# Optimization experiments

Hardware: AMD Instinct MI355X
Metric: run time of the kernel (lower is better)

The kernel has to match this reference:

```python
import jax, jax.numpy as jnp
import numpy as np

HEADS = 4


def rel_to_abs(x):
    """Convert relative logits [..., L, 2L-1] to absolute [..., L, L].
    out[..., i, j] = x[..., i, j - i + L - 1]."""
    L = x.shape[-2]
    idx = jnp.arange(L)[None, :] - jnp.arange(L)[:, None] + (L - 1)  # [L, L]
    idx = jnp.broadcast_to(idx, x.shape[:-1] + (L,))
    return jnp.take_along_axis(x, idx, axis=-1)


def setup_inputs() -> dict:
    key = jax.random.key(0)
    ks = jax.random.split(key, 5)
    b, c, h, w = 2, 256, 64, 64
    dh = c // HEADS
    return {
        "x": jax.random.normal(ks[0], (b, c, h, w), jnp.float32),
        "w_qkv": jax.random.normal(ks[1], (3 * c, c), jnp.float32) / np.float32(np.sqrt(c)),
        "w_out": jax.random.normal(ks[2], (c, c), jnp.float32) / np.float32(np.sqrt(c)),
        "rel_height": jax.random.normal(ks[3], (2 * h - 1, dh), jnp.float32),
        "rel_width": jax.random.normal(ks[4], (2 * w - 1, dh), jnp.float32),
    }


def reference(x, w_qkv, w_out, rel_height, rel_width):
    b, c, h, w = x.shape
    dh = c // HEADS
    N = h * w
    scale = dh ** -0.5

    # 1x1 conv == per-pixel matmul over channels
    qkv = jnp.einsum('bchw,oc->bohw', x, w_qkv)  # [b, 3c, h, w]
    q, k, v = jnp.split(qkv, 3, axis=1)

    def to_heads(t):  # [b, c, h, w] -> [b, H, N, dh]
        return t.reshape(b, HEADS, dh, N).transpose(0, 1, 3, 2)

    q = to_heads(q) * scale
    k = to_heads(k)
    v = to_heads(v)

    # content-content scores over spatial positions
    content = jnp.einsum('bnid,bnjd->bnij', q, k)  # [b, H, N, N]

    q5 = q.reshape(b, HEADS, h, w, dh)  # [b, H, x, y, dh]
    # width relative logits: [b,H,x,y,2w-1] -> abs -> [b,H,x,y,jw]
    rw = rel_to_abs(jnp.einsum('bnxyd,rd->bnxyr', q5, rel_width))
    # height relative logits on transposed spatial: [b,H,y,x,2h-1] -> [b,H,y,x,jh]
    rh = rel_to_abs(jnp.einsum('bnyxd,rd->bnyxr', q5.transpose(0, 1, 3, 2, 4), rel_height))

    logits = content.reshape(b, HEADS, h, w, h, w)
    logits = logits + rw[:, :, :, :, None, :]  # broadcast width bias over target height jh
    logits = logits + rh.transpose(0, 1, 3, 2, 4)[:, :, :, :, :, None]  # [b,H,x,y,jh] over jw

    attn = jax.nn.softmax(logits.reshape(b, HEADS, N, N), axis=-1)
    out = jnp.einsum('bnij,bnjd->bnid', attn, v)  # [b, H, N, dh]
    out = out.transpose(0, 1, 3, 2).reshape(b, c, h, w)
    out = jnp.einsum('bchw,oc->bohw', out, w_out)  # 1x1 out projection
    return out + x
```

## Files before the change

### kernel.cpp

```cpp
#include <hip/hip_runtime.h>

typedef unsigned short u16;
typedef unsigned int u32;
typedef __bf16 bf16x8 __attribute__((ext_vector_type(8)));
typedef __bf16 bf16x2 __attribute__((ext_vector_type(2)));
typedef float f32x4 __attribute__((ext_vector_type(4)));
typedef float f32x2 __attribute__((ext_vector_type(2)));
typedef u32 u32x4 __attribute__((ext_vector_type(4)));
typedef u32 u32x2 __attribute__((ext_vector_type(2)));

#define DEVI __device__ __forceinline__

#if defined(__has_builtin)
#if __has_builtin(__builtin_amdgcn_exp2f)
#define EXP2F(x) __builtin_amdgcn_exp2f(x)
#endif
#endif
#ifndef EXP2F
#define EXP2F(x) exp2f(x)
#endif

#define MFMA16(a, b, c) __builtin_amdgcn_mfma_f32_16x16x32_bf16(a, b, c, 0, 0, 0)

typedef __attribute__((address_space(1))) u32 gu32;
typedef __attribute__((address_space(3))) u32 lu32;
DEVI void gll16(const u16* g, u16* l) {
    __builtin_amdgcn_global_load_lds((const gu32*)g, (lu32*)l, 16, 0, 0);
}
#define WAIT_VM0() __builtin_amdgcn_s_waitcnt(0x0f70)

DEVI u16 f2bf(float f) {
    u32 u = __builtin_bit_cast(u32, f);
    u = (u + 0x7FFFu + ((u >> 16) & 1u)) >> 16;
    return (u16)u;
}
DEVI float bf2f(u16 h) {
    u32 u = ((u32)h) << 16;
    return __builtin_bit_cast(float, u);
}
DEVI float bfhi(u32 u) { return __builtin_bit_cast(float, u & 0xFFFF0000u); }
DEVI float bflo(u32 u) { return __builtin_bit_cast(float, u << 16); }
DEVI bf16x8 bc8(u32x4 u) { return __builtin_bit_cast(bf16x8, u); }
DEVI u32 pack2(float a, float b) {
    f32x2 v = {a, b};
    bf16x2 h = __builtin_convertvector(v, bf16x2);
    return __builtin_bit_cast(u32, h);
}

#define QSCALE 0.18033688011112042f

__global__ __launch_bounds__(256) void k_prep(const float* __restrict__ x,
                                              const float* __restrict__ wq,
                                              const float* __restrict__ wo,
                                              const float* __restrict__ relh,
                                              const float* __restrict__ relw,
                                              u16* __restrict__ xt, u16* __restrict__ wqb,
                                              u16* __restrict__ wob, u16* __restrict__ relhb,
                                              u16* __restrict__ relwb) {
    int bid = blockIdx.x;
    int t = threadIdx.x;
    if (bid < 512) {
        int pm = bid & 63, cm = (bid >> 6) & 3, b = bid >> 8;
        int p0 = pm * 64, c0 = cm * 64;
        __shared__ float tile[64][65];
#pragma unroll
        for (int it = 0; it < 4; ++it) {
            int idx = it * 256 + t;
            int cl = idx >> 4, f4 = idx & 15;
            f32x4 v = *(const f32x4*)(x + ((size_t)(b * 256 + c0 + cl)) * 4096 + p0 + f4 * 4);
            tile[cl][f4 * 4 + 0] = v[0];
            tile[cl][f4 * 4 + 1] = v[1];
            tile[cl][f4 * 4 + 2] = v[2];
            tile[cl][f4 * 4 + 3] = v[3];
        }
        __syncthreads();
#pragma unroll
        for (int it = 0; it < 2; ++it) {
            int idx = it * 256 + t;
            int pl = idx >> 3, g = idx & 7;
            u32x4 pk;
            pk.x = pack2(tile[g * 8 + 0][pl], tile[g * 8 + 1][pl]);
            pk.y = pack2(tile[g * 8 + 2][pl], tile[g * 8 + 3][pl]);
            pk.z = pack2(tile[g * 8 + 4][pl], tile[g * 8 + 5][pl]);
            pk.w = pack2(tile[g * 8 + 6][pl], tile[g * 8 + 7][pl]);
            *(u32x4*)(xt + ((size_t)(b * 4096 + p0 + pl)) * 256 + c0 + g * 8) = pk;
        }
    } else {
        int i0 = (bid - 512) * 256 + t;
#pragma unroll
        for (int i = i0; i < 196608; i += 65536) wqb[i] = f2bf(wq[i]);
        if (i0 < 65536) wob[i0] = f2bf(wo[i0]);
        if (i0 < 8192) {
            relhb[i0] = (i0 < 8128) ? f2bf(relh[i0]) : (u16)0;
            relwb[i0] = (i0 < 8128) ? f2bf(relw[i0]) : (u16)0;
        }
    }
}

__global__ __launch_bounds__(256) void k_qkv(const u16* __restrict__ xt, const u16* __restrict__ wqb,
                                             const u16* __restrict__ relwb,
                                             const u16* __restrict__ relhb,
                                             u16* __restrict__ q, u16* __restrict__ k,
                                             u16* __restrict__ vt, u16* __restrict__ Wabs,
                                             u16* __restrict__ HabsT) {
    int pm = blockIdx.x, on = blockIdx.y, b = blockIdx.z;
    int p0 = pm * 64, o0 = on * 64;
    __shared__ __align__(16) u16 Sm[64 * 256];
    int t = threadIdx.x;
    int wv = t >> 6, l = t & 63, quad = l >> 4, li = l & 15;

    u32x4 areg[8];
    const u32x4* arow = (const u32x4*)(xt + ((size_t)(b * 4096 + p0 + wv * 16 + li)) * 256);
#pragma unroll
    for (int kc = 0; kc < 8; ++kc) areg[kc] = arow[kc * 4 + quad];

    {
        int pc = l & 31;
#pragma unroll
        for (int i = 0; i < 8; ++i) {
            int r = wv * 16 + i * 2 + (l >> 5);
            gll16(wqb + (size_t)(o0 + r) * 256 + ((pc + r) & 31) * 8,
                  Sm + (wv * 16 + i * 2) * 256);
        }
    }
    WAIT_VM0();
    __syncthreads();

    f32x4 acc[4] = {{0, 0, 0, 0}, {0, 0, 0, 0}, {0, 0, 0, 0}, {0, 0, 0, 0}};
#pragma unroll
    for (int kc = 0; kc < 8; ++kc) {
        bf16x8 a = bc8(areg[kc]);
#pragma unroll
        for (int ct = 0; ct < 4; ++ct) {
            bf16x8 bb = bc8(*(const u32x4*)(Sm + (ct * 16 + li) * 256 +
                                            (((kc * 4 + quad) - (ct * 16 + li)) & 31) * 8));
            acc[ct] = MFMA16(a, bb, acc[ct]);
        }
    }

    int tensor = on >> 2, head = on & 3;
    if (tensor == 2) {
        __syncthreads();
        u16* T = Sm;
#pragma unroll
        for (int ct = 0; ct < 4; ++ct)
#pragma unroll
            for (int r = 0; r < 4; ++r)
                T[(ct * 16 + li) * 72 + wv * 16 + quad * 4 + r] = f2bf(acc[ct][r]);
        __syncthreads();
        int dr = t >> 2, pc = (t & 3) * 16;
        u32x4* g = (u32x4*)(vt + ((size_t)((b * 4 + head) * 64 + dr)) * 4096 + p0 + pc);
        const u32x4* s2 = (const u32x4*)(T + dr * 72 + pc);
        g[0] = s2[0];
        g[1] = s2[1];
    } else {
        u16* outp = (tensor == 0) ? q : k;
        float sc = (tensor == 0) ? QSCALE : 1.0f;
#pragma unroll
        for (int ct = 0; ct < 4; ++ct)
#pragma unroll
            for (int r = 0; r < 4; ++r) {
                int p = p0 + wv * 16 + quad * 4 + r;
                int d = ct * 16 + li;
                outp[((size_t)((b * 4 + head) * 4096 + p)) * 64 + d] = f2bf(acc[ct][r] * sc);
            }
        if (tensor == 0) {
            int bh = b * 4 + head;
            u16* T = Sm;
            u16* Ls = Sm + 64 * 72;
            __syncthreads();
#pragma unroll
            for (int ct = 0; ct < 4; ++ct)
#pragma unroll
                for (int r = 0; r < 4; ++r)
                    T[(wv * 16 + quad * 4 + r) * 72 + ct * 16 + li] = f2bf(acc[ct][r] * QSCALE);
            {
                int row = t >> 1, half = t & 1;
                const u32x4* g2 = (const u32x4*)(relwb + row * 64 + half * 32);
                u32x4* s2 = (u32x4*)(Ls + row * 72 + half * 32);
#pragma unroll
                for (int kk = 0; kk < 4; ++kk) s2[kk] = g2[kk];
            }
            __syncthreads();
            u32x4 aq2[2];
            aq2[0] = *(const u32x4*)(T + (wv * 16 + li) * 72 + quad * 8);
            aq2[1] = *(const u32x4*)(T + (wv * 16 + li) * 72 + 32 + quad * 8);

            f32x4 acc2[8];
#pragma unroll
            for (int ct = 0; ct < 8; ++ct) acc2[ct] = (f32x4){0.f, 0.f, 0.f, 0.f};
#pragma unroll
            for (int kc = 0; kc < 2; ++kc) {
                bf16x8 a = bc8(aq2[kc]);
#pragma unroll
                for (int ct = 0; ct < 8; ++ct) {
                    bf16x8 bb = bc8(*(const u32x4*)(Ls + (ct * 16 + li) * 72 + kc * 32 + quad * 8));
                    acc2[ct] = MFMA16(a, bb, acc2[ct]);
                }
            }
#pragma unroll
            for (int ct = 0; ct < 8; ++ct)
#pragma unroll
                for (int r = 0; r < 4; ++r) {
                    int row = wv * 16 + quad * 4 + r;
                    int j = (ct * 16 + li) - 63 + row;
                    if (j >= 0 && j < 64)
                        Wabs[((size_t)(bh * 4096 + p0 + row)) * 64 + j] = f2bf(acc2[ct][r]);
                }
            __syncthreads();
            {
                int row = t >> 1, half = t & 1;
                const u32x4* g2 = (const u32x4*)(relhb + row * 64 + half * 32);
                u32x4* s2 = (u32x4*)(Ls + row * 72 + half * 32);
#pragma unroll
                for (int kk = 0; kk < 4; ++kk) s2[kk] = g2[kk];
            }
            __syncthreads();
#pragma unroll
            for (int ct = 0; ct < 8; ++ct) acc2[ct] = (f32x4){0.f, 0.f, 0.f, 0.f};
#pragma unroll
            for (int kc = 0; kc < 2; ++kc) {
                bf16x8 a = bc8(aq2[kc]);
#pragma unroll
                for (int ct = 0; ct < 8; ++ct) {
                    bf16x8 bb = bc8(*(const u32x4*)(Ls + (ct * 16 + li) * 72 + kc * 32 + quad * 8));
                    acc2[ct] = MFMA16(a, bb, acc2[ct]);
                }
            }
#pragma unroll
            for (int ct = 0; ct < 8; ++ct)
#pragma unroll
                for (int r = 0; r < 4; ++r) {
                    int row = wv * 16 + quad * 4 + r;
                    int j = (ct * 16 + li) - 63 + pm;
                    if (j >= 0 && j < 64)
                        HabsT[((size_t)(bh * 64 + j)) * 4096 + p0 + row] = f2bf(acc2[ct][r]);
                }
        }
    }
}

__global__ __launch_bounds__(256, 2) void k_flash(const u16* __restrict__ q,
                                                  const u16* __restrict__ kg,
                                                  const u16* __restrict__ vt,
                                                  const u16* __restrict__ Wabs,
                                                  const u16* __restrict__ HabsT,
                                                  u16* __restrict__ OP,
                                                  float* __restrict__ LS) {
    int pm = blockIdx.x, bh = blockIdx.y, ks = blockIdx.z;
    int p0 = pm * 256;
    __shared__ __align__(16) u16 Kt[2][64 * 64];
    __shared__ __align__(16) u16 Vl[2][64 * 64];
    int t = threadIdx.x, wv = t >> 6, l = t & 63, quad = l >> 4, li = l & 15;
    int rbase = wv * 64;

    u32x4 aq[4][2];
#pragma unroll
    for (int rs = 0; rs < 4; ++rs) {
        const u32x4* qrow =
            (const u32x4*)(q + ((size_t)(bh * 4096 + p0 + rbase + rs * 16 + li)) * 64);
        aq[rs][0] = qrow[quad];
        aq[rs][1] = qrow[4 + quad];
    }

    u32x2 wbp[4][4];
#pragma unroll
    for (int rs = 0; rs < 4; ++rs)
#pragma unroll
        for (int ct = 0; ct < 4; ++ct) {
            int jcol = ((ct >> 1) * 32) + quad * 8 + ((ct & 1) * 4);
            const u32* wp = (const u32*)(Wabs +
                                         ((size_t)(bh * 4096 + p0 + rbase + rs * 16 + li)) * 64 +
                                         jcol);
            wbp[rs][ct] = (u32x2){wp[0], wp[1]};
        }

    const u16* hbase = HabsT + ((size_t)(bh * 64 + ks * 16)) * 4096 + p0 + rbase;

    int ln3 = l >> 3, ln7 = l & 7;
    int xo = (ln7 ^ ln3) * 8;
    int R0 = wv * 8 + ln3, R1 = 32 + R0;
    int j0r = (R0 & 32) | ((R0 & 16) >> 2) | ((R0 & 8) << 1) | ((R0 & 4) << 1) | (R0 & 3);
    int j1r = (R1 & 32) | ((R1 & 16) >> 2) | ((R1 & 8) << 1) | ((R1 & 4) << 1) | (R1 & 3);
    const u16* kS0 = kg + ((size_t)(bh * 4096 + ks * 1024 + j0r)) * 64 + xo;
    const u16* kS1 = kg + ((size_t)(bh * 4096 + ks * 1024 + j1r)) * 64 + xo;
    const u16* vS0 = vt + ((size_t)(bh * 64 + R0)) * 4096 + ks * 1024 + xo;
    const u16* vS1 = vt + ((size_t)(bh * 64 + R1)) * 4096 + ks * 1024 + xo;
    int ldst = wv * 512;

    int o0 = li * 64 + ((quad ^ ln7) * 8);
    int o1 = li * 64 + (((quad + 4) ^ ln7) * 8);

    gll16(kS0, Kt[0] + ldst);
    gll16(kS1, Kt[0] + 2048 + ldst);
    gll16(vS0, Vl[0] + ldst);
    gll16(vS1, Vl[0] + 2048 + ldst);
    u16 hc[4];
#pragma unroll
    for (int rs = 0; rs < 4; ++rs) hc[rs] = hbase[rs * 16 + li];
    WAIT_VM0();

    f32x4 oacc[4][5];
#pragma unroll
    for (int rs = 0; rs < 4; ++rs)
#pragma unroll
        for (int ct = 0; ct < 5; ++ct) oacc[rs][ct] = (f32x4){0.f, 0.f, 0.f, 0.f};

    const u32x4 ones = {0x3F803F80u, 0x3F803F80u, 0x3F803F80u, 0x3F803F80u};

    for (int kt = 0; kt < 16; ++kt) {
        __syncthreads();
        int cur = kt & 1;
        const u16* Kc = Kt[cur];
        const u16* Vc = Vl[cur];
        u16 hn[4];
        if (kt < 15) {
            kS0 += 4096;
            kS1 += 4096;
            vS0 += 64;
            vS1 += 64;
            u16* Kn = Kt[cur ^ 1];
            u16* Vn = Vl[cur ^ 1];
            gll16(kS0, Kn + ldst);
            gll16(kS1, Kn + 2048 + ldst);
            gll16(vS0, Vn + ldst);
            gll16(vS1, Vn + 2048 + ldst);
#pragma unroll
            for (int rs = 0; rs < 4; ++rs) hn[rs] = hbase[(size_t)(kt + 1) * 4096 + rs * 16 + li];
        }

        u32x4 pf[4][2];
#pragma unroll
        for (int ct = 0; ct < 4; ++ct) {
            bf16x8 af0 = bc8(*(const u32x4*)(Kc + ct * 1024 + o0));
            bf16x8 af1 = bc8(*(const u32x4*)(Kc + ct * 1024 + o1));
#pragma unroll
            for (int rs = 0; rs < 4; ++rs) {
                float hh = bf2f(hc[rs]);
                u32x2 w = wbp[rs][ct];
                f32x4 s4 = {bflo(w.x) + hh, bfhi(w.x) + hh, bflo(w.y) + hh, bfhi(w.y) + hh};
                s4 = MFMA16(af0, bc8(aq[rs][0]), s4);
                s4 = MFMA16(af1, bc8(aq[rs][1]), s4);
                u32 pa = pack2(EXP2F(s4[0]), EXP2F(s4[1]));
                u32 pb = pack2(EXP2F(s4[2]), EXP2F(s4[3]));
                if (ct & 1) {
                    pf[rs][ct >> 1].z = pa;
                    pf[rs][ct >> 1].w = pb;
                } else {
                    pf[rs][ct >> 1].x = pa;
                    pf[rs][ct >> 1].y = pb;
                }
            }
        }

        __builtin_amdgcn_s_setprio(1);
#pragma unroll
        for (int dt = 0; dt < 4; ++dt) {
            bf16x8 B0 = bc8(*(const u32x4*)(Vc + dt * 1024 + o0));
            bf16x8 B1 = bc8(*(const u32x4*)(Vc + dt * 1024 + o1));
#pragma unroll
            for (int rs = 0; rs < 4; ++rs) {
                oacc[rs][dt] = MFMA16(bc8(pf[rs][0]), B0, oacc[rs][dt]);
                oacc[rs][dt] = MFMA16(bc8(pf[rs][1]), B1, oacc[rs][dt]);
            }
        }
#pragma unroll
        for (int rs = 0; rs < 4; ++rs) {
            oacc[rs][4] = MFMA16(bc8(pf[rs][0]), bc8(ones), oacc[rs][4]);
            oacc[rs][4] = MFMA16(bc8(pf[rs][1]), bc8(ones), oacc[rs][4]);
        }
        __builtin_amdgcn_s_setprio(0);

        if (kt < 15) {
            WAIT_VM0();
#pragma unroll
            for (int rs = 0; rs < 4; ++rs) hc[rs] = hn[rs];
        }
    }

#pragma unroll
    for (int rs = 0; rs < 4; ++rs) {
#pragma unroll
        for (int ct = 0; ct < 4; ++ct)
#pragma unroll
            for (int r = 0; r < 4; ++r) {
                int p = p0 + rbase + rs * 16 + quad * 4 + r;
                OP[((size_t)((ks * 8 + bh) * 4096 + p)) * 64 + ct * 16 + li] =
                    f2bf(oacc[rs][ct][r]);
            }
        if (li == 0) {
#pragma unroll
            for (int r = 0; r < 4; ++r) {
                int p = p0 + rbase + rs * 16 + quad * 4 + r;
                LS[(size_t)(ks * 8 + bh) * 4096 + p] = oacc[rs][4][r];
            }
        }
    }
}

__global__ __launch_bounds__(256) void k_out2(const u16* __restrict__ wob,
                                              const u16* __restrict__ OP,
                                              const float* __restrict__ LS,
                                              const float* __restrict__ x,
                                              float* __restrict__ out) {
    int pm = blockIdx.x, b = blockIdx.y, coh = blockIdx.z;
    int p0 = pm * 32;
    __shared__ __align__(16) u16 Bt[32 * 264];
    int t = threadIdx.x, wv = t >> 6, l = t & 63, quad = l >> 4, li = l & 15;

    {
        int row = t >> 3, head = (t >> 1) & 3, hf = t & 1;
        int bh = b * 4 + head;
        int p = p0 + row;
        const u32x4* o0p = (const u32x4*)(OP + ((size_t)(bh * 4096 + p)) * 64) + hf * 4;
        const u32x4* o1p = (const u32x4*)(OP + ((size_t)((8 + bh) * 4096 + p)) * 64) + hf * 4;
        const u32x4* o2p = (const u32x4*)(OP + ((size_t)((16 + bh) * 4096 + p)) * 64) + hf * 4;
        const u32x4* o3p = (const u32x4*)(OP + ((size_t)((24 + bh) * 4096 + p)) * 64) + hf * 4;
        float linv = 1.0f / (LS[(size_t)bh * 4096 + p] + LS[(size_t)(8 + bh) * 4096 + p] +
                             LS[(size_t)(16 + bh) * 4096 + p] + LS[(size_t)(24 + bh) * 4096 + p]);
        u16* dst = Bt + row * 264 + head * 64 + hf * 32;
#pragma unroll
        for (int kk = 0; kk < 4; ++kk) {
            u32x4 a = o0p[kk], c = o1p[kk], d = o2p[kk], e = o3p[kk];
            u32x4 pk;
            pk.x = pack2((bflo(a.x) + bflo(c.x) + bflo(d.x) + bflo(e.x)) * linv,
                         (bfhi(a.x) + bfhi(c.x) + bfhi(d.x) + bfhi(e.x)) * linv);
            pk.y = pack2((bflo(a.y) + bflo(c.y) + bflo(d.y) + bflo(e.y)) * linv,
                         (bfhi(a.y) + bfhi(c.y) + bfhi(d.y) + bfhi(e.y)) * linv);
            pk.z = pack2((bflo(a.z) + bflo(c.z) + bflo(d.z) + bflo(e.z)) * linv,
                         (bfhi(a.z) + bfhi(c.z) + bfhi(d.z) + bfhi(e.z)) * linv);
            pk.w = pack2((bflo(a.w) + bflo(c.w) + bflo(d.w) + bflo(e.w)) * linv,
                         (bfhi(a.w) + bfhi(c.w) + bfhi(d.w) + bfhi(e.w)) * linv);
            *(u32x4*)(dst + kk * 8) = pk;
        }
    }
    __syncthreads();

#pragma unroll
    for (int ci = 0; ci < 2; ++ci) {
        int com = coh * 2 + ci;
        int co0 = com * 64;
        f32x4 acc[2] = {{0, 0, 0, 0}, {0, 0, 0, 0}};
        const u32x4* arow = (const u32x4*)(wob + (size_t)(co0 + wv * 16 + li) * 256);
#pragma unroll
        for (int kc = 0; kc < 8; ++kc) {
            bf16x8 a = bc8(arow[kc * 4 + quad]);
#pragma unroll
            for (int ct = 0; ct < 2; ++ct) {
                bf16x8 bb = bc8(*(const u32x4*)(Bt + (ct * 16 + li) * 264 + kc * 32 + quad * 8));
                acc[ct] = MFMA16(a, bb, acc[ct]);
            }
        }
#pragma unroll
        for (int ct = 0; ct < 2; ++ct)
#pragma unroll
            for (int r = 0; r < 4; ++r) {
                size_t idx =
                    ((size_t)(b * 256 + co0 + wv * 16 + quad * 4 + r)) * 4096 + p0 + ct * 16 + li;
                out[idx] = acc[ct][r] + x[idx];
            }
    }
}

extern "C" void kernel_launch(void* const* d_in, const int* in_sizes, int n_in, void* d_out,
                              int out_size, void* d_ws, size_t ws_size, hipStream_t stream) {
    const float* x = (const float*)d_in[0];
    const float* wqkv = (const float*)d_in[1];
    const float* wout = (const float*)d_in[2];
    const float* relh = (const float*)d_in[3];
    const float* relw = (const float*)d_in[4];
    float* out = (float*)d_out;
    char* ws = (char*)d_ws;

    u16* xt = (u16*)(ws + 0);
    u16* wqb = (u16*)(ws + 4194304);
    u16* wob = (u16*)(ws + 4587520);
    u16* relwb = (u16*)(ws + 4718592);
    u16* relhb = (u16*)(ws + 4734976);
    u16* qb = (u16*)(ws + 4751360);
    u16* kb = (u16*)(ws + 8945664);
    u16* vtb = (u16*)(ws + 13139968);
    u16* Wabs = (u16*)(ws + 17334272);
    u16* HabsT = (u16*)(ws + 21528576);
    u16* OPart = (u16*)(ws + 25722880);
    float* LSum = (float*)(ws + 0);

    k_prep<<<768, 256, 0, stream>>>(x, wqkv, wout, relh, relw, xt, wqb, wob, relhb, relwb);
    k_qkv<<<dim3(64, 12, 2), 256, 0, stream>>>(xt, wqb, relwb, relhb, qb, kb, vtb, Wabs, HabsT);
    k_flash<<<dim3(16, 8, 4), 256, 0, stream>>>(qb, kb, vtb, Wabs, HabsT, OPart, LSum);
    k_out2<<<dim3(128, 2, 2), 256, 0, stream>>>(wob, OPart, LSum, x, out);
}
```

Before: 136.1 us.

## Software-pipeline attention loop to overlap next QK with current PV

Restructures the attention main loop into a two-stage software pipeline. The loop is unrolled by two, and the QK^T/exp for the next key tile is computed while the PV MFMAs for the previous tile are issued. K and V loads are staggered across double buffers so that K runs one tile ahead of V. This is meant to hide exp/VALU latency behind MFMA work and overlap global loads. The cost is higher register pressure from two live P fragment sets and more intricate buffer synchronization.

```diff
diff --git a/kernel.cpp b/kernel.cpp
--- a/kernel.cpp
+++ b/kernel.cpp
@@ -291,15 +291,6 @@
     int o0 = li * 64 + ((quad ^ ln7) * 8);
     int o1 = li * 64 + (((quad + 4) ^ ln7) * 8);
 
-    gll16(kS0, Kt[0] + ldst);
-    gll16(kS1, Kt[0] + 2048 + ldst);
-    gll16(vS0, Vl[0] + ldst);
-    gll16(vS1, Vl[0] + 2048 + ldst);
-    u16 hc[4];
-#pragma unroll
-    for (int rs = 0; rs < 4; ++rs) hc[rs] = hbase[rs * 16 + li];
-    WAIT_VM0();
-
     f32x4 oacc[4][5];
 #pragma unroll
     for (int rs = 0; rs < 4; ++rs)
@@ -308,35 +299,14 @@
 
     const u32x4 ones = {0x3F803F80u, 0x3F803F80u, 0x3F803F80u, 0x3F803F80u};
 
-    for (int kt = 0; kt < 16; ++kt) {
-        __syncthreads();
-        int cur = kt & 1;
-        const u16* Kc = Kt[cur];
-        const u16* Vc = Vl[cur];
-        u16 hn[4];
-        if (kt < 15) {
-            kS0 += 4096;
-            kS1 += 4096;
-            vS0 += 64;
-            vS1 += 64;
-            u16* Kn = Kt[cur ^ 1];
-            u16* Vn = Vl[cur ^ 1];
-            gll16(kS0, Kn + ldst);
-            gll16(kS1, Kn + 2048 + ldst);
-            gll16(vS0, Vn + ldst);
-            gll16(vS1, Vn + 2048 + ldst);
-#pragma unroll
-            for (int rs = 0; rs < 4; ++rs) hn[rs] = hbase[(size_t)(kt + 1) * 4096 + rs * 16 + li];
-        }
-
-        u32x4 pf[4][2];
+    auto QKf = [&](const u16* Kc, const u16* hq, u32x4 (&pf)[4][2]) {
 #pragma unroll
         for (int ct = 0; ct < 4; ++ct) {
             bf16x8 af0 = bc8(*(const u32x4*)(Kc + ct * 1024 + o0));
             bf16x8 af1 = bc8(*(const u32x4*)(Kc + ct * 1024 + o1));
 #pragma unroll
             for (int rs = 0; rs < 4; ++rs) {
-                float hh = bf2f(hc[rs]);
+                float hh = bf2f(hq[rs]);
                 u32x2 w = wbp[rs][ct];
                 f32x4 s4 = {bflo(w.x) + hh, bfhi(w.x) + hh, bflo(w.y) + hh, bfhi(w.y) + hh};
                 s4 = MFMA16(af0, bc8(aq[rs][0]), s4);
@@ -352,7 +322,8 @@
                 }
             }
         }
-
+    };
+    auto PVf = [&](const u32x4 (&pf)[4][2], const u16* Vc) {
         __builtin_amdgcn_s_setprio(1);
 #pragma unroll
         for (int dt = 0; dt < 4; ++dt) {
@@ -370,12 +341,73 @@
             oacc[rs][4] = MFMA16(bc8(pf[rs][1]), bc8(ones), oacc[rs][4]);
         }
         __builtin_amdgcn_s_setprio(0);
-
-        if (kt < 15) {
-            WAIT_VM0();
-#pragma unroll
-            for (int rs = 0; rs < 4; ++rs) hc[rs] = hn[rs];
-        }
+    };
+
+    gll16(kS0, Kt[0] + ldst);
+    gll16(kS1, Kt[0] + 2048 + ldst);
+    gll16(vS0, Vl[0] + ldst);
+    gll16(vS1, Vl[0] + 2048 + ldst);
+    u16 h0[4], hn[4];
+#pragma unroll
+    for (int rs = 0; rs < 4; ++rs) h0[rs] = hbase[rs * 16 + li];
+    WAIT_VM0();
+    __syncthreads();
+    kS0 += 4096;
+    kS1 += 4096;
+    gll16(kS0, Kt[1] + ldst);
+    gll16(kS1, Kt[1] + 2048 + ldst);
+#pragma unroll
+    for (int rs = 0; rs < 4; ++rs) hn[rs] = hbase[(size_t)4096 + rs * 16 + li];
+
+    u32x4 pfA[4][2], pfB[4][2];
+    QKf(Kt[0], h0, pfA);
+
+    for (int kt2 = 0; kt2 < 8; ++kt2) {
+        int kte = kt2 * 2;
+        WAIT_VM0();
+        __syncthreads();
+        {
+            u16 hq[4];
+#pragma unroll
+            for (int rs = 0; rs < 4; ++rs) hq[rs] = hn[rs];
+            if (kte < 14) {
+                kS0 += 4096;
+                kS1 += 4096;
+                gll16(kS0, Kt[0] + ldst);
+                gll16(kS1, Kt[0] + 2048 + ldst);
+            }
+            vS0 += 64;
+            vS1 += 64;
+            gll16(vS0, Vl[1] + ldst);
+            gll16(vS1, Vl[1] + 2048 + ldst);
+            if (kte < 14) {
+#pragma unroll
+                for (int rs = 0; rs < 4; ++rs)
+                    hn[rs] = hbase[(size_t)(kte + 2) * 4096 + rs * 16 + li];
+            }
+            QKf(Kt[1], hq, pfB);
+            PVf(pfA, Vl[0]);
+        }
+        WAIT_VM0();
+        __syncthreads();
+        if (kte < 14) {
+            u16 hq[4];
+#pragma unroll
+            for (int rs = 0; rs < 4; ++rs) hq[rs] = hn[rs];
+            kS0 += 4096;
+            kS1 += 4096;
+            gll16(kS0, Kt[1] + ldst);
+            gll16(kS1, Kt[1] + 2048 + ldst);
+            vS0 += 64;
+            vS1 += 64;
+            gll16(vS0, Vl[0] + ldst);
+            gll16(vS1, Vl[0] + 2048 + ldst);
+#pragma unroll
+            for (int rs = 0; rs < 4; ++rs)
+                hn[rs] = hbase[(size_t)(kte + 3) * 4096 + rs * 16 + li];
+            QKf(Kt[0], hq, pfA);
+        }
+        PVf(pfB, Vl[1]);
     }
 
 #pragma unroll
```

Measured after the change: 228.9 us. +68.2%, slower.
